# Kernel optimization log

Hardware: AMD Instinct MI355X
Metric: run time of the kernel (lower is better)

The kernel has to match this reference:

```python
import jax, jax.numpy as jnp
from jax import lax
import numpy as np

PH, PW = 5, 5      # patch_shape; forced to 5x5 by the (batch, F, 27) reshape in AdaptiveConv
F = 32             # adaptive conv output channels
SCALE = 4          # super-resolution upscale factor


def conv2d(x, w, b, padding):
    # x: NCHW, w: OIHW
    y = lax.conv_general_dilated(x, w, (1, 1), padding,
                                 dimension_numbers=('NCHW', 'OIHW', 'NCHW'))
    return y + b[None, :, None, None]


def space_to_batch(x):
    # non-overlapping PHxPW tiles, order (batch, tile_row, tile_col) like the torch loops
    B, C, H, W = x.shape
    hn, wn = H // PH, W // PW
    p = x.reshape(B, C, hn, PH, wn, PW).transpose(0, 2, 4, 1, 3, 5)
    return p.reshape(B * hn * wn, C, PH, PW), (B, hn, wn)


def batch_to_space(p, meta):
    B, hn, wn = meta
    C = p.shape[1]
    out = p.reshape(B, hn, wn, C, PH, PW).transpose(0, 3, 1, 4, 2, 5)
    return out.reshape(B, C, hn * PH, wn * PW)


def unfold3(x):
    # torch F.unfold(x, 3, padding=1): (N, C*9, L) channel-major (c, kh, kw); return (N, L, C*9)
    N, C, H, W = x.shape
    xp = jnp.pad(x, ((0, 0), (0, 0), (1, 1), (1, 1)))
    cols = jnp.stack([xp[:, :, i:i + H, j:j + W]
                      for i in range(3) for j in range(3)], axis=2)  # (N, C, 9, H, W)
    return cols.reshape(N, C * 9, H * W).transpose(0, 2, 1)


def pixel_shuffle(x, r):
    B, Cr2, H, W = x.shape
    C = Cr2 // (r * r)
    return (x.reshape(B, C, r, r, H, W)
             .transpose(0, 1, 4, 2, 5, 3)
             .reshape(B, C, H * r, W * r))


def setup_inputs() -> dict:
    key = jax.random.key(0)
    ks = jax.random.split(key, 13)
    rn = lambda k, shape, s=0.05: jax.random.normal(k, shape, jnp.float32) * s
    return dict(
        x=jax.random.normal(ks[0], (2, 3, 360, 640), jnp.float32),
        w_feat=rn(ks[1], (256, 3, 3, 3)),        b_feat=rn(ks[2], (256,)),
        w_kern=rn(ks[3], (27 * F, 256, 3, 3)),   b_kern=rn(ks[4], (27 * F,)),
        w_badp=rn(ks[5], (F, 256, 3, 3)),        b_badp=rn(ks[6], (F,)),
        w1=rn(ks[7], (128, F, 5, 5)),            b1=rn(ks[8], (128,)),
        w2=rn(ks[9], (32, 128, 3, 3)),           b2=rn(ks[10], (32,)),
        w3=rn(ks[11], (3 * SCALE * SCALE, 32, 3, 3)), b3=rn(ks[12], (3 * SCALE * SCALE,)),
    )


def reference(x, w_feat, b_feat, w_kern, b_kern, w_badp, b_badp,
              w1, b1, w2, b2, w3, b3):
    patches, meta = space_to_batch(x)                        # (N, 3, 5, 5)
    N = patches.shape[0]
    # AdaptiveConv: per-patch dynamic 3x3 conv
    feat = jax.nn.relu(conv2d(patches, w_feat, b_feat, 'VALID'))   # (N, 256, 3, 3)
    kern = conv2d(feat, w_kern, b_kern, 'VALID')                   # (N, 27F, 1, 1)
    kern = kern.reshape(N, F, 27).transpose(0, 2, 1)               # (N, 27, F)
    xu = unfold3(patches)                                          # (N, 25, 27)
    out = jnp.einsum('nlk,nkf->nlf', xu, kern)                     # (N, 25, F)
    out = out.transpose(0, 2, 1).reshape(N, F, PH, PW)
    bias = conv2d(feat, w_badp, b_badp, 'VALID')                   # (N, F, 1, 1)
    out = jax.nn.relu(out + bias)
    sp = batch_to_space(out, meta)                                 # (B, F, H, W)
    # RegularConv stack
    h = jax.nn.relu(conv2d(sp, w1, b1, 'SAME'))
    h = jax.nn.relu(conv2d(h, w2, b2, 'SAME'))
    h = conv2d(h, w3, b3, 'SAME')                                  # (B, 3*r*r, H, W)
    return pixel_shuffle(h, SCALE)                                 # (B, 3, H*r, W*r)
```

## Files before the change

kernel.cpp:

```cpp
#include <hip/hip_runtime.h>
#include <stdint.h>

typedef unsigned short ushort;
typedef __bf16 bf16x8 __attribute__((ext_vector_type(8)));
typedef float f32x4 __attribute__((ext_vector_type(4)));
typedef ushort ushort8 __attribute__((ext_vector_type(8)));
typedef ushort us4 __attribute__((ext_vector_type(4)));

__device__ __forceinline__ float bf2f(ushort u) {
  union { unsigned int i; float f; } v; v.i = ((unsigned int)u) << 16; return v.f;
}
__device__ __forceinline__ ushort f2bf(float f) {
  union { float f; unsigned int i; } v; v.f = f;
  unsigned int r = v.i + 0x7fffu + ((v.i >> 16) & 1u);
  return (ushort)(r >> 16);
}
__device__ __forceinline__ void glds16(const ushort* g, ushort* l) {
  __builtin_amdgcn_global_load_lds(
      (const __attribute__((address_space(1))) void*)g,
      (__attribute__((address_space(3))) void*)l, 16, 0, 0);
}
__device__ __forceinline__ bf16x8 ldw(const ushort* p) {
  return __builtin_bit_cast(bf16x8, *(const ushort8*)p);
}

__global__ __launch_bounds__(256) void pack_kernel(
    const float* __restrict__ w_kern, const float* __restrict__ b_kern,
    const float* __restrict__ w_badp, const float* __restrict__ b_badp,
    ushort* __restrict__ Bt, float* __restrict__ bias896) {
  int idx = blockIdx.x * 256 + threadIdx.x;
  const int total = 896 * 2304;
  if (idx < total) {
    int o = idx / 2304, k = idx - o * 2304;
    int c = k & 255, pos = k >> 8;
    float v = (o < 864) ? w_kern[(o * 256 + c) * 9 + pos]
                        : w_badp[((o - 864) * 256 + c) * 9 + pos];
    Bt[idx] = f2bf(v);
  } else if (idx < total + 896) {
    int o = idx - total;
    bias896[o] = (o < 864) ? b_kern[o] : b_badp[o - 864];
  }
}

__global__ __launch_bounds__(256) void pack2_kernel(
    const float* __restrict__ w1, const float* __restrict__ w2,
    const float* __restrict__ w3, ushort* __restrict__ wp1,
    ushort* __restrict__ wp2, ushort* __restrict__ wp3) {
  int idx = blockIdx.x * 256 + threadIdx.x;
  if (idx < 102400) {
    int t = idx >> 12, rm = idx & 4095, o = rm >> 5, c = rm & 31;
    wp1[idx] = f2bf(w1[(o * 32 + c) * 25 + t]);
  } else if (idx < 102400 + 36864) {
    int j = idx - 102400;
    int t = j >> 12, rm = j & 4095, o = rm >> 7, c = rm & 127;
    wp2[j] = f2bf(w2[(o * 128 + c) * 9 + t]);
  } else if (idx < 102400 + 36864 + 13824) {
    int j = idx - 139264;
    int t = j / 1536, rm = j - t * 1536, o = rm >> 5, c = rm & 31;
    wp3[j] = f2bf(w3[(o * 32 + c) * 9 + t]);
  }
}

__global__ __launch_bounds__(256) void feat_kernel(
    const float* __restrict__ x, const float* __restrict__ w_feat,
    const float* __restrict__ b_feat, ushort* __restrict__ feat) {
  __shared__ float xp[4][3][5][5];
  const int t = threadIdx.x;
  const int n0 = blockIdx.x * 4;
  for (int e = t; e < 300; e += 256) {
    int p = e / 75, rem = e - p * 75;
    int ci = rem / 25, r = rem - ci * 25, i = r / 5, j = r - i * 5;
    int n = n0 + p;
    int b = n / 9216, ph = (n >> 7) % 72, pw = n & 127;
    xp[p][ci][i][j] = x[((b * 3 + ci) * 360 + ph * 5 + i) * 640 + pw * 5 + j];
  }
  float wf[27];
#pragma unroll
  for (int m = 0; m < 27; ++m) wf[m] = w_feat[t * 27 + m];
  const float bv = b_feat[t];
  __syncthreads();
  for (int p = 0; p < 4; ++p) {
    ushort* dst = feat + (size_t)(n0 + p) * 2304 + t;
#pragma unroll
    for (int pi = 0; pi < 3; ++pi)
#pragma unroll
      for (int pj = 0; pj < 3; ++pj) {
        float acc = bv;
#pragma unroll
        for (int ci = 0; ci < 3; ++ci)
#pragma unroll
          for (int ki = 0; ki < 3; ++ki)
#pragma unroll
            for (int kj = 0; kj < 3; ++kj)
              acc = fmaf(xp[p][ci][pi + ki][pj + kj], wf[ci * 9 + ki * 3 + kj], acc);
        dst[(pi * 3 + pj) * 256] = f2bf(fmaxf(acc, 0.f));
      }
  }
}

__global__ __launch_bounds__(256) void gemm_kernel(
    const ushort* __restrict__ A, const ushort* __restrict__ Bt,
    const float* __restrict__ bias, ushort* __restrict__ C) {
  const int K = 2304, N = 896;
  __shared__ __align__(16) ushort lA[128 * 32];
  __shared__ __align__(16) ushort lB[128 * 32];
  const int m0 = blockIdx.x * 128, n0 = blockIdx.y * 128;
  const int t = threadIdx.x;
  const int lane = t & 63, wave = t >> 6;
  const int wm = wave >> 1, wn = wave & 1;
  f32x4 acc[4][4] = {};
  const ushort* gA = A + (size_t)(m0 + (t >> 2)) * K + (t & 3) * 8;
  const ushort* gB = Bt + (size_t)(n0 + (t >> 2)) * K + (t & 3) * 8;
  ushort* dA0 = &lA[wave * 512];
  ushort* dA1 = &lA[2048 + wave * 512];
  ushort* dB0 = &lB[wave * 512];
  ushort* dB1 = &lB[2048 + wave * 512];
  const int aoff = (wm * 64 + (lane & 15)) * 32 + (lane >> 4) * 8;
  const int boff = (wn * 64 + (lane & 15)) * 32 + (lane >> 4) * 8;
  for (int kt = 0; kt < K; kt += 32) {
    __syncthreads();
    glds16(gA + kt, dA0);
    glds16(gA + 64 * K + kt, dA1);
    glds16(gB + kt, dB0);
    glds16(gB + 64 * K + kt, dB1);
    __syncthreads();
    bf16x8 af[4], bfr[4];
#pragma unroll
    for (int mi = 0; mi < 4; ++mi) {
      ushort8 tmp = *(const ushort8*)(&lA[aoff + mi * 512]);
      af[mi] = __builtin_bit_cast(bf16x8, tmp);
    }
#pragma unroll
    for (int ni = 0; ni < 4; ++ni) {
      ushort8 tmp = *(const ushort8*)(&lB[boff + ni * 512]);
      bfr[ni] = __builtin_bit_cast(bf16x8, tmp);
    }
#pragma unroll
    for (int mi = 0; mi < 4; ++mi)
#pragma unroll
      for (int ni = 0; ni < 4; ++ni)
        acc[mi][ni] = __builtin_amdgcn_mfma_f32_16x16x32_bf16(af[mi], bfr[ni], acc[mi][ni], 0, 0, 0);
  }
#pragma unroll
  for (int ni = 0; ni < 4; ++ni) {
    int col = n0 + wn * 64 + ni * 16 + (lane & 15);
    float bv = bias[col];
#pragma unroll
    for (int mi = 0; mi < 4; ++mi) {
      int row0 = m0 + wm * 64 + mi * 16 + (lane >> 4) * 4;
#pragma unroll
      for (int r = 0; r < 4; ++r)
        C[(size_t)(row0 + r) * N + col] = f2bf(acc[mi][ni][r] + bv);
    }
  }
}

__global__ __launch_bounds__(256) void apply_kernel(
    const float* __restrict__ x, const ushort* __restrict__ kernbias,
    ushort* __restrict__ sp) {
  __shared__ float xp[8][3][7][7];
  __shared__ ushort outl[8][32][25];
  const int t = threadIdx.x;
  const int n0 = blockIdx.x * 8;
  const int b = n0 / 9216, ph = (n0 >> 7) % 72, pw0 = n0 & 127;
  for (int e = t; e < 8 * 3 * 49; e += 256) ((float*)xp)[e] = 0.f;
  __syncthreads();
  for (int e = t; e < 600; e += 256) {
    int p = e / 75, rem = e - p * 75;
    int ci = rem / 25, r = rem - ci * 25, i = r / 5, j = r - i * 5;
    xp[p][ci][i + 1][j + 1] = x[((b * 3 + ci) * 360 + ph * 5 + i) * 640 + (pw0 + p) * 5 + j];
  }
  __syncthreads();
  const int p = t >> 5, f = t & 31;
  const int n = n0 + p;
  float kk[27];
#pragma unroll
  for (int k = 0; k < 27; ++k) kk[k] = bf2f(kernbias[(size_t)n * 896 + f * 27 + k]);
  const float bv = bf2f(kernbias[(size_t)n * 896 + 864 + f]);
  for (int l = 0; l < 25; ++l) {
    int li = l / 5, lj = l - li * 5;
    float s = bv;
#pragma unroll
    for (int k = 0; k < 27; ++k) {
      int ci = k / 9, rm = k - ci * 9, ki = rm / 3, kj = rm - ki * 3;
      s = fmaf(xp[p][ci][li + ki][lj + kj], kk[k], s);
    }
    outl[p][f][l] = f2bf(fmaxf(s, 0.f));
  }
  __syncthreads();
  for (int e = t; e < 6400; e += 256) {
    int f2 = e & 31;
    int idx = e >> 5;
    int i = idx / 40, c40 = idx - i * 40;
    int pp = c40 / 5, j = c40 - pp * 5;
    sp[(((size_t)b * 360 + ph * 5 + i) * 640 + pw0 * 5 + c40) * 32 + f2] = outl[pp][f2][i * 5 + j];
  }
}

__global__ __launch_bounds__(512) void conv1_kernel(
    const ushort* __restrict__ sp, const ushort* __restrict__ wp1,
    const float* __restrict__ b1, ushort* __restrict__ h1) {
  __shared__ ushort8 lin[8 * 4 * 69];
  const int t = threadIdx.x;
  const int lane = t & 63, wave = t >> 6;
  const int wh = wave >> 1, wn = wave & 1;
  const int w0 = blockIdx.x * 64, h0 = blockIdx.y * 4, b = blockIdx.z;
  for (int u = t; u < 8 * 4 * 68; u += 512) {
    int c8 = u & 3, rest = u >> 2;
    int wx = rest % 68, r = rest / 68;
    int gh = h0 - 2 + r, gw = w0 - 2 + wx;
    ushort8 v = {};
    if ((unsigned)gh < 360u && (unsigned)gw < 640u)
      v = *(const ushort8*)(sp + (((size_t)b * 360 + gh) * 640 + gw) * 32 + c8 * 8);
    lin[(r * 4 + c8) * 69 + wx] = v;
  }
  __syncthreads();
  f32x4 acc[4][4] = {};
  const int lp = lane & 15, lk = lane >> 4;
  const int abase0 = lk * 69 + lp;
  const ushort* wb = wp1 + (wn * 64 + lp) * 32 + lk * 8;

  bf16x8 wc[4], wx_[4];
#pragma unroll
  for (int nf = 0; nf < 4; ++nf) wc[nf] = ldw(wb + nf * 512);

  auto do_tap = [&](int tp, const bf16x8* wr) {
    int ki = (tp * 13) >> 6, kj = tp - ki * 5;
    int ab = (wh + ki) * 276 + abase0 + kj;
    bf16x8 afr[4];
#pragma unroll
    for (int mf = 0; mf < 4; ++mf)
      afr[mf] = __builtin_bit_cast(bf16x8, lin[ab + mf * 16]);
#pragma unroll
    for (int mf = 0; mf < 4; ++mf)
#pragma unroll
      for (int nf = 0; nf < 4; ++nf)
        acc[mf][nf] = __builtin_amdgcn_mfma_f32_16x16x32_bf16(wr[nf], afr[mf], acc[mf][nf], 0, 0, 0);
  };

#pragma unroll 1
  for (int tp = 0; tp < 24; tp += 2) {
#pragma unroll
    for (int nf = 0; nf < 4; ++nf) wx_[nf] = ldw(wb + (tp + 1) * 4096 + nf * 512);
    do_tap(tp, wc);
#pragma unroll
    for (int nf = 0; nf < 4; ++nf) wc[nf] = ldw(wb + (tp + 2) * 4096 + nf * 512);
    do_tap(tp + 1, wx_);
  }
  do_tap(24, wc);

  const int h = h0 + wh;
#pragma unroll
  for (int nf = 0; nf < 4; ++nf) {
    const int oc0 = wn * 64 + nf * 16 + lk * 4;
    f32x4 bv = *(const f32x4*)(b1 + oc0);
#pragma unroll
    for (int mf = 0; mf < 4; ++mf) {
      const int w = w0 + mf * 16 + lp;
      us4 pk;
#pragma unroll
      for (int r = 0; r < 4; ++r) pk[r] = f2bf(fmaxf(acc[mf][nf][r] + bv[r], 0.f));
      *(us4*)(&h1[(((size_t)b * 360 + h) * 640 + w) * 128 + oc0]) = pk;
    }
  }
}

__device__ __forceinline__ void c2_load(ushort8* stg, const ushort* __restrict__ h1,
                                        int t, int b, int h0, int w0, int cb) {
#pragma unroll
  for (int j = 0; j < 7; ++j) {
    int u = t + j * 256;
    ushort8 v = {};
    if (u < 1584) {
      int r = u / 264, rem = u - r * 264;
      int c8 = rem / 66, wx = rem - c8 * 66;
      int gh = h0 - 1 + r, gw = w0 - 1 + wx;
      if ((unsigned)gh < 360u && (unsigned)gw < 640u)
        v = *(const ushort8*)(h1 + (((size_t)b * 360 + gh) * 640 + gw) * 128 + cb * 32 + c8 * 8);
    }
    stg[j] = v;
  }
}
__device__ __forceinline__ void c2_write(const ushort8* stg, ushort8* buf, int t) {
#pragma unroll
  for (int j = 0; j < 7; ++j) {
    int u = t + j * 256;
    if (u < 1584) {
      int r = u / 264, rem = u - r * 264;
      int c8 = rem / 66, wx = rem - c8 * 66;
      buf[c8 * 414 + r * 69 + wx] = stg[j];
    }
  }
}
__device__ __forceinline__ void c2_compute(const ushort8* buf, const ushort* __restrict__ wp2,
                                           int cb, int wave, int lp, int lk, f32x4 acc[4][2]) {
#pragma unroll
  for (int ki = 0; ki < 3; ++ki) {
    const int rb = lk * 414 + (wave + ki) * 69;
#pragma unroll
    for (int kj = 0; kj < 3; ++kj) {
      const int tap = ki * 3 + kj;
      bf16x8 bfr[2];
#pragma unroll
      for (int nf = 0; nf < 2; ++nf) {
        ushort8 tmp = *(const ushort8*)(wp2 + tap * 4096 + nf * 2048 + lp * 128 + cb * 32 + lk * 8);
        bfr[nf] = __builtin_bit_cast(bf16x8, tmp);
      }
      bf16x8 afr[4];
#pragma unroll
      for (int mf = 0; mf < 4; ++mf)
        afr[mf] = __builtin_bit_cast(bf16x8, buf[rb + lp + mf * 16 + kj]);
#pragma unroll
      for (int mf = 0; mf < 4; ++mf)
#pragma unroll
        for (int nf = 0; nf < 2; ++nf)
          acc[mf][nf] = __builtin_amdgcn_mfma_f32_16x16x32_bf16(bfr[nf], afr[mf], acc[mf][nf], 0, 0, 0);
    }
  }
}

__global__ __launch_bounds__(256) void conv2_kernel(
    const ushort* __restrict__ h1, const ushort* __restrict__ wp2,
    const float* __restrict__ b2, ushort* __restrict__ h2) {
  __shared__ ushort8 lin[2][4 * 414];
  const int t = threadIdx.x;
  const int lane = t & 63, wave = t >> 6;
  const int lp = lane & 15, lk = lane >> 4;
  const int w0 = blockIdx.x * 64, h0 = blockIdx.y * 4, b = blockIdx.z;
  f32x4 acc[4][2] = {};
  ushort8 stg[7];
  c2_load(stg, h1, t, b, h0, w0, 0);
#pragma unroll
  for (int it = 0; it < 5; ++it) {
    __syncthreads();
    if (it < 4) c2_write(stg, lin[it & 1], t);
    if (it < 3) c2_load(stg, h1, t, b, h0, w0, it + 1);
    if (it >= 1) c2_compute(lin[(it - 1) & 1], wp2, it - 1, wave, lp, lk, acc);
  }
  const int h = h0 + wave;
#pragma unroll
  for (int nf = 0; nf < 2; ++nf) {
    const int oc0 = nf * 16 + lk * 4;
    f32x4 bv = *(const f32x4*)(b2 + oc0);
#pragma unroll
    for (int mf = 0; mf < 4; ++mf) {
      const int w = w0 + mf * 16 + lp;
      us4 pk;
#pragma unroll
      for (int r = 0; r < 4; ++r) pk[r] = f2bf(fmaxf(acc[mf][nf][r] + bv[r], 0.f));
      *(us4*)(&h2[(((size_t)b * 360 + h) * 640 + w) * 32 + oc0]) = pk;
    }
  }
}

__global__ __launch_bounds__(256) void conv3_kernel(
    const ushort* __restrict__ h2, const ushort* __restrict__ wp3,
    const float* __restrict__ b3, float* __restrict__ out) {
  __shared__ ushort8 lin[4 * 4 * 67];
  const int t = threadIdx.x;
  const int lane = t & 63, wave = t >> 6;
  const int wh = wave & 1, wm = wave >> 1;
  const int lp = lane & 15, lk = lane >> 4;
  const int w0 = blockIdx.x * 64, h0 = blockIdx.y * 2, b = blockIdx.z;
  for (int u = t; u < 4 * 4 * 66; u += 256) {
    int c8 = u & 3, rest = u >> 2;
    int wx = rest % 66, r = rest / 66;
    int gh = h0 - 1 + r, gw = w0 - 1 + wx;
    ushort8 v = {};
    if (gh >= 0 && gh < 360 && gw >= 0 && gw < 640)
      v = *(const ushort8*)(h2 + (((size_t)b * 360 + gh) * 640 + gw) * 32 + c8 * 8);
    lin[(r * 4 + c8) * 67 + wx] = v;
  }
  __syncthreads();
  f32x4 acc[2][3] = {};
  const int abase = lk * 67 + wm * 32 + lp;
  const ushort* wbase = wp3 + lp * 32 + lk * 8;
#pragma unroll 1
  for (int ki = 0; ki < 3; ++ki) {
#pragma unroll
    for (int kj = 0; kj < 3; ++kj) {
      const int tap = ki * 3 + kj;
      bf16x8 bfr[3];
#pragma unroll
      for (int nf = 0; nf < 3; ++nf) {
        ushort8 tmp = *(const ushort8*)(wbase + (size_t)tap * 1536 + nf * 512);
        bfr[nf] = __builtin_bit_cast(bf16x8, tmp);
      }
      bf16x8 afr[2];
#pragma unroll
      for (int mf = 0; mf < 2; ++mf)
        afr[mf] = __builtin_bit_cast(bf16x8, lin[(wh + ki) * 268 + abase + mf * 16 + kj]);
#pragma unroll
      for (int mf = 0; mf < 2; ++mf)
#pragma unroll
        for (int nf = 0; nf < 3; ++nf)
          acc[mf][nf] = __builtin_amdgcn_mfma_f32_16x16x32_bf16(bfr[nf], afr[mf], acc[mf][nf], 0, 0, 0);
    }
  }
  const int h = h0 + wh;
#pragma unroll
  for (int nf = 0; nf < 3; ++nf) {
    f32x4 bv = *(const f32x4*)(b3 + nf * 16 + lk * 4);
#pragma unroll
    for (int mf = 0; mf < 2; ++mf) {
      const int w = w0 + wm * 32 + mf * 16 + lp;
      f32x4 o;
#pragma unroll
      for (int r = 0; r < 4; ++r) o[r] = acc[mf][nf][r] + bv[r];
      *(f32x4*)(&out[(((size_t)b * 3 + nf) * 1440 + h * 4 + lk) * 2560 + (size_t)w * 4]) = o;
    }
  }
}

extern "C" void kernel_launch(void* const* d_in, const int* in_sizes, int n_in,
                              void* d_out, int out_size, void* d_ws, size_t ws_size,
                              hipStream_t stream) {
  const float* x      = (const float*)d_in[0];
  const float* w_feat = (const float*)d_in[1];
  const float* b_feat = (const float*)d_in[2];
  const float* w_kern = (const float*)d_in[3];
  const float* b_kern = (const float*)d_in[4];
  const float* w_badp = (const float*)d_in[5];
  const float* b_badp = (const float*)d_in[6];
  const float* w1 = (const float*)d_in[7];
  const float* b1 = (const float*)d_in[8];
  const float* w2 = (const float*)d_in[9];
  const float* b2 = (const float*)d_in[10];
  const float* w3 = (const float*)d_in[11];
  const float* b3 = (const float*)d_in[12];

  char* ws = (char*)d_ws;
  ushort* feat     = (ushort*)(ws);
  ushort* h1       = (ushort*)(ws);
  ushort* kernbias = (ushort*)(ws + 117964800);
  ushort* h2       = (ushort*)(ws + 117964800);
  ushort* wp1      = (ushort*)(ws + 147456000);
  ushort* wp2      = (ushort*)(ws + 147660800);
  ushort* wp3      = (ushort*)(ws + 147734528);
  ushort* sp       = (ushort*)(ws + 150994944);
  ushort* Bt       = (ushort*)(ws + 180486144);
  float*  bias896  = (float*)(ws + 184614912);

  pack_kernel<<<(896 * 2304 + 896 + 255) / 256, 256, 0, stream>>>(
      w_kern, b_kern, w_badp, b_badp, Bt, bias896);
  feat_kernel<<<4608, 256, 0, stream>>>(x, w_feat, b_feat, feat);
  gemm_kernel<<<dim3(144, 7), 256, 0, stream>>>(feat, Bt, bias896, kernbias);
  apply_kernel<<<2304, 256, 0, stream>>>(x, kernbias, sp);
  pack2_kernel<<<598, 256, 0, stream>>>(w1, w2, w3, wp1, wp2, wp3);
  conv1_kernel<<<dim3(10, 90, 2), 512, 0, stream>>>(sp, wp1, b1, h1);
  conv2_kernel<<<dim3(10, 90, 2), 256, 0, stream>>>(h1, wp2, b2, h2);
  conv3_kernel<<<dim3(10, 180, 2), 256, 0, stream>>>(h2, wp3, b3, (float*)d_out);
}
```

Baseline: 512.3 us.

## Stage conv1 weights in LDS, remap GEMM blocks per XCD, unroll conv3

```diff
diff --git a/kernel.cpp b/kernel.cpp
--- a/kernel.cpp
+++ b/kernel.cpp
@@ -19,9 +19,6 @@
   __builtin_amdgcn_global_load_lds(
       (const __attribute__((address_space(1))) void*)g,
       (__attribute__((address_space(3))) void*)l, 16, 0, 0);
-}
-__device__ __forceinline__ bf16x8 ldw(const ushort* p) {
-  return __builtin_bit_cast(bf16x8, *(const ushort8*)p);
 }
 
 __global__ __launch_bounds__(256) void pack_kernel(
@@ -104,7 +101,10 @@
   const int K = 2304, N = 896;
   __shared__ __align__(16) ushort lA[128 * 32];
   __shared__ __align__(16) ushort lB[128 * 32];
-  const int m0 = blockIdx.x * 128, n0 = blockIdx.y * 128;
+  const int bid = blockIdx.x;
+  const int xcd = bid & 7, j = bid >> 3;
+  const int mblk = xcd * 18 + j / 7, nblk = j % 7;
+  const int m0 = mblk * 128, n0 = nblk * 128;
   const int t = threadIdx.x;
   const int lane = t & 63, wave = t >> 6;
   const int wm = wave >> 1, wn = wave & 1;
@@ -197,13 +197,15 @@
   }
 }
 
-__global__ __launch_bounds__(512) void conv1_kernel(
+__global__ __launch_bounds__(512, 4) void conv1_kernel(
     const ushort* __restrict__ sp, const ushort* __restrict__ wp1,
     const float* __restrict__ b1, ushort* __restrict__ h1) {
   __shared__ ushort8 lin[8 * 4 * 69];
+  __shared__ ushort8 wbuf[2][1024];
   const int t = threadIdx.x;
   const int lane = t & 63, wave = t >> 6;
   const int wh = wave >> 1, wn = wave & 1;
+  const int lp = lane & 15, lk = lane >> 4;
   const int w0 = blockIdx.x * 64, h0 = blockIdx.y * 4, b = blockIdx.z;
   for (int u = t; u < 8 * 4 * 68; u += 512) {
     int c8 = u & 3, rest = u >> 2;
@@ -214,40 +216,33 @@
       v = *(const ushort8*)(sp + (((size_t)b * 360 + gh) * 640 + gw) * 32 + c8 * 8);
     lin[(r * 4 + c8) * 69 + wx] = v;
   }
-  __syncthreads();
+  ushort* wd0 = (ushort*)&wbuf[0][wave * 64];
+  ushort* wd1 = (ushort*)&wbuf[1][wave * 64];
+  glds16(wp1 + t * 8, wd0);
+  __syncthreads();
+
   f32x4 acc[4][4] = {};
-  const int lp = lane & 15, lk = lane >> 4;
-  const int abase0 = lk * 69 + lp;
-  const ushort* wb = wp1 + (wn * 64 + lp) * 32 + lk * 8;
-
-  bf16x8 wc[4], wx_[4];
-#pragma unroll
-  for (int nf = 0; nf < 4; ++nf) wc[nf] = ldw(wb + nf * 512);
-
-  auto do_tap = [&](int tp, const bf16x8* wr) {
-    int ki = (tp * 13) >> 6, kj = tp - ki * 5;
-    int ab = (wh + ki) * 276 + abase0 + kj;
-    bf16x8 afr[4];
+#pragma unroll
+  for (int tp = 0; tp < 25; ++tp) {
+    if (tp < 24)
+      glds16(wp1 + (tp + 1) * 4096 + t * 8, ((tp + 1) & 1) ? wd1 : wd0);
+    const int ki = tp / 5, kj = tp % 5;
+    const ushort8* wb8 = wbuf[tp & 1];
+    bf16x8 W[4], Af[4];
+#pragma unroll
+    for (int nf = 0; nf < 4; ++nf)
+      W[nf] = __builtin_bit_cast(bf16x8, wb8[(wn * 64 + nf * 16 + lp) * 4 + lk]);
+    const int ab = (wh + ki) * 276 + lk * 69 + lp + kj;
 #pragma unroll
     for (int mf = 0; mf < 4; ++mf)
-      afr[mf] = __builtin_bit_cast(bf16x8, lin[ab + mf * 16]);
+      Af[mf] = __builtin_bit_cast(bf16x8, lin[ab + mf * 16]);
 #pragma unroll
     for (int mf = 0; mf < 4; ++mf)
 #pragma unroll
       for (int nf = 0; nf < 4; ++nf)
-        acc[mf][nf] = __builtin_amdgcn_mfma_f32_16x16x32_bf16(wr[nf], afr[mf], acc[mf][nf], 0, 0, 0);
-  };
-
-#pragma unroll 1
-  for (int tp = 0; tp < 24; tp += 2) {
-#pragma unroll
-    for (int nf = 0; nf < 4; ++nf) wx_[nf] = ldw(wb + (tp + 1) * 4096 + nf * 512);
-    do_tap(tp, wc);
-#pragma unroll
-    for (int nf = 0; nf < 4; ++nf) wc[nf] = ldw(wb + (tp + 2) * 4096 + nf * 512);
-    do_tap(tp + 1, wx_);
-  }
-  do_tap(24, wc);
+        acc[mf][nf] = __builtin_amdgcn_mfma_f32_16x16x32_bf16(W[nf], Af[mf], acc[mf][nf], 0, 0, 0);
+    if (tp < 24) __syncthreads();
+  }
 
   const int h = h0 + wh;
 #pragma unroll
@@ -375,7 +370,7 @@
   f32x4 acc[2][3] = {};
   const int abase = lk * 67 + wm * 32 + lp;
   const ushort* wbase = wp3 + lp * 32 + lk * 8;
-#pragma unroll 1
+#pragma unroll
   for (int ki = 0; ki < 3; ++ki) {
 #pragma unroll
     for (int kj = 0; kj < 3; ++kj) {
@@ -444,7 +439,7 @@
   pack_kernel<<<(896 * 2304 + 896 + 255) / 256, 256, 0, stream>>>(
       w_kern, b_kern, w_badp, b_badp, Bt, bias896);
   feat_kernel<<<4608, 256, 0, stream>>>(x, w_feat, b_feat, feat);
-  gemm_kernel<<<dim3(144, 7), 256, 0, stream>>>(feat, Bt, bias896, kernbias);
+  gemm_kernel<<<1008, 256, 0, stream>>>(feat, Bt, bias896, kernbias);
   apply_kernel<<<2304, 256, 0, stream>>>(x, kernbias, sp);
   pack2_kernel<<<598, 256, 0, stream>>>(w1, w2, w3, wp1, wp2, wp3);
   conv1_kernel<<<dim3(10, 90, 2), 512, 0, stream>>>(sp, wp1, b1, h1);
```

After: 469.6 us. 1.09x faster.
